# Optimization experiments

Hardware: AMD Instinct MI355X
Metric: run time of the kernel (lower is better)

Reference implementation:

```python
import jax, jax.numpy as jnp
import numpy as np


def setup_inputs() -> dict:
    key = jax.random.key(0)
    k1, k2, k3, k4 = jax.random.split(key, 4)
    N, M, D = 4096, 4096, 8
    x = jax.random.normal(k1, (N, D), dtype=jnp.float32)
    xx = jax.random.normal(k2, (M, D), dtype=jnp.float32)
    # raw (free-form) hyperparameters; positive() = softplus
    scale_raw = jax.random.normal(k3, (D,), dtype=jnp.float32)
    variance_raw = jax.random.normal(k4, (), dtype=jnp.float32)
    return {"x": x, "xx": xx, "scale_raw": scale_raw, "variance_raw": variance_raw}


def reference(x, xx, scale_raw, variance_raw):
    scale = jax.nn.softplus(scale_raw)          # (D,)
    variance = jax.nn.softplus(variance_raw)    # scalar
    xs = x / scale                               # (N, D)
    xxs = xx / scale                             # (M, D)
    # squared euclidean distance without materializing (N, M, D):
    # ||a-b||^2 = ||a||^2 + ||b||^2 - 2 a.b
    sq_x = jnp.sum(xs * xs, axis=-1)             # (N,)
    sq_xx = jnp.sum(xxs * xxs, axis=-1)          # (M,)
    cross = jnp.einsum("nd,md->nm", xs, xxs)    # (N, M)
    d2 = jnp.maximum(sq_x[:, None] + sq_xx[None, :] - 2.0 * cross, 0.0)
    cov = jnp.exp(-0.5 * d2) * variance          # (N, M)
    return cov
```

## Files before the change

kernel.cpp:

```cpp
#include <hip/hip_runtime.h>
#include <math.h>


#define TILE_N 16
#define BLOCK 256
#define D 8
#define M_PER_BLOCK (BLOCK * 4)

typedef float v2f __attribute__((ext_vector_type(2)));
typedef float v4f __attribute__((ext_vector_type(4)));

__device__ __forceinline__ float softplus_f(float z) {
    return fmaxf(z, 0.0f) + log1pf(__expf(-fabsf(z)));
}

__device__ __forceinline__ float fast_exp2(float z) {
    return __builtin_exp2f(z);
}

__global__ __launch_bounds__(BLOCK) void rbf_kernel(
    const float* __restrict__ x,
    const float* __restrict__ xx,
    const float* __restrict__ scale_raw,
    const float* __restrict__ var_raw,
    float* __restrict__ out,
    int N, int M)
{
    __shared__ float s_a[TILE_N][D];
    __shared__ float s_c[TILE_N];
    __shared__ float s_rs[D];
    __shared__ float s_l2v;

    const int tid = threadIdx.x;
    const int m0 = blockIdx.x * M_PER_BLOCK + tid * 4;
    const int n0 = blockIdx.y * TILE_N;

    if (tid < D) {
        s_rs[tid] = 1.2011224087864498f / softplus_f(scale_raw[tid]);
    }
    if (tid == D) {
        s_l2v = log2f(softplus_f(var_raw[0]));
    }
    __syncthreads();

    if (tid < TILE_N * D) {
        const int r = tid >> 3, c = tid & 7;
        s_a[r][c] = x[(n0 + r) * D + c] * s_rs[c];
    }

    float rs[D];
#pragma unroll
    for (int d = 0; d < D; ++d) rs[d] = s_rs[d];

    v2f b01[D], b23[D];
    {
        const float* xxp = xx + (size_t)m0 * D;
        float bj[4][D];
#pragma unroll
        for (int j = 0; j < 4; ++j) {
            const float4 lo = *(const float4*)(xxp + j * D);
            const float4 hi = *(const float4*)(xxp + j * D + 4);
            bj[j][0] = lo.x * rs[0]; bj[j][1] = lo.y * rs[1];
            bj[j][2] = lo.z * rs[2]; bj[j][3] = lo.w * rs[3];
            bj[j][4] = hi.x * rs[4]; bj[j][5] = hi.y * rs[5];
            bj[j][6] = hi.z * rs[6]; bj[j][7] = hi.w * rs[7];
        }
#pragma unroll
        for (int d = 0; d < D; ++d) {
            b01[d] = (v2f){bj[0][d], bj[1][d]};
            b23[d] = (v2f){bj[2][d], bj[3][d]};
        }
    }
    v2f h01 = {0.f, 0.f}, h23 = {0.f, 0.f};
#pragma unroll
    for (int d = 0; d < D; ++d) {
        h01 = __builtin_elementwise_fma(b01[d], b01[d], h01);
        h23 = __builtin_elementwise_fma(b23[d], b23[d], h23);
    }
    h01 *= 0.5f; h23 *= 0.5f;

    __syncthreads();

    if (tid < TILE_N) {
        float s = 0.f;
#pragma unroll
        for (int d = 0; d < D; ++d) s = fmaf(s_a[tid][d], s_a[tid][d], s);
        s_c[tid] = s_l2v - 0.5f * s;
    }
    __syncthreads();

    const float l2v = s_l2v;

#pragma unroll
    for (int n = 0; n < TILE_N; ++n) {
        const float4 alo = *(const float4*)&s_a[n][0];
        const float4 ahi = *(const float4*)&s_a[n][4];
        const float c = s_c[n];
        const float a_[D] = {alo.x, alo.y, alo.z, alo.w, ahi.x, ahi.y, ahi.z, ahi.w};

        v2f acc01 = (v2f){c, c} - h01;
        v2f acc23 = (v2f){c, c} - h23;
#pragma unroll
        for (int d = 0; d < D; ++d) {
            const v2f av = (v2f){a_[d], a_[d]};
            acc01 = __builtin_elementwise_fma(av, b01[d], acc01);
            acc23 = __builtin_elementwise_fma(av, b23[d], acc23);
        }

        v4f r;
        r.x = fast_exp2(fminf(acc01.x, l2v));
        r.y = fast_exp2(fminf(acc01.y, l2v));
        r.z = fast_exp2(fminf(acc23.x, l2v));
        r.w = fast_exp2(fminf(acc23.y, l2v));
        __builtin_nontemporal_store(r, (v4f*)(out + (size_t)(n0 + n) * M + m0));
    }
}

extern "C" void kernel_launch(void* const* d_in, const int* in_sizes, int n_in,
                              void* d_out, int out_size, void* d_ws, size_t ws_size,
                              hipStream_t stream) {
    const float* x    = (const float*)d_in[0];
    const float* xx   = (const float*)d_in[1];
    const float* sraw = (const float*)d_in[2];
    const float* vraw = (const float*)d_in[3];
    float* out = (float*)d_out;

    const int N = in_sizes[0] / D;
    const int M = in_sizes[1] / D;

    dim3 grid(M / M_PER_BLOCK, N / TILE_N);
    rbf_kernel<<<grid, BLOCK, 0, stream>>>(x, xx, sraw, vraw, out, N, M);
}
```

Baseline: 88.35 us.

## Reshape RBF tile to 8 rows x 8 columns per thread and drop a block barrier

Changes the per-thread tile from 4 columns by 16 rows to 8 columns by 8 rows, so each thread issues two contiguous float4 stores per row. Every thread now computes the softplus scales itself with fast hardware intrinsics, which removes the shared-memory broadcast and one __syncthreads. Row norms are computed in parallel with the row loading, and launch bounds ask for 4 blocks per CU. Register use goes up, and the store pattern has 32-byte strided chunks per thread instead of 16-byte ones, which may change how well writes coalesce.

```diff
diff --git a/kernel.cpp b/kernel.cpp
--- a/kernel.cpp
+++ b/kernel.cpp
@@ -2,23 +2,23 @@
 #include <math.h>
 
 
-#define TILE_N 16
+#define TILE_N 8
+#define D 8
 #define BLOCK 256
-#define D 8
-#define M_PER_BLOCK (BLOCK * 4)
+#define M_PER_T 8
+#define M_PER_BLOCK (BLOCK * M_PER_T)
 
 typedef float v2f __attribute__((ext_vector_type(2)));
 typedef float v4f __attribute__((ext_vector_type(4)));
 
-__device__ __forceinline__ float softplus_f(float z) {
-    return fmaxf(z, 0.0f) + log1pf(__expf(-fabsf(z)));
+__device__ __forceinline__ float fast_softplus(float z) {
+    const float LOG2E = 1.4426950408889634f;
+    const float LN2   = 0.6931471805599453f;
+    const float t = __builtin_amdgcn_exp2f(-fabsf(z) * LOG2E);
+    return fmaxf(z, 0.0f) + LN2 * __builtin_amdgcn_logf(1.0f + t);
 }
 
-__device__ __forceinline__ float fast_exp2(float z) {
-    return __builtin_exp2f(z);
-}
-
-__global__ __launch_bounds__(BLOCK) void rbf_kernel(
+__global__ __launch_bounds__(BLOCK, 4) void rbf_kernel(
     const float* __restrict__ x,
     const float* __restrict__ xx,
     const float* __restrict__ scale_raw,
@@ -28,91 +28,114 @@
 {
     __shared__ float s_a[TILE_N][D];
     __shared__ float s_c[TILE_N];
-    __shared__ float s_rs[D];
-    __shared__ float s_l2v;
 
     const int tid = threadIdx.x;
-    const int m0 = blockIdx.x * M_PER_BLOCK + tid * 4;
+    const int m0 = blockIdx.x * M_PER_BLOCK + tid * M_PER_T;
     const int n0 = blockIdx.y * TILE_N;
 
-    if (tid < D) {
-        s_rs[tid] = 1.2011224087864498f / softplus_f(scale_raw[tid]);
+    const float SQ_L2E = 1.2011224087864498f;
+
+    float rs[D];
+    {
+        const float4 s0 = *(const float4*)(scale_raw);
+        const float4 s1 = *(const float4*)(scale_raw + 4);
+        rs[0] = SQ_L2E * __builtin_amdgcn_rcpf(fast_softplus(s0.x));
+        rs[1] = SQ_L2E * __builtin_amdgcn_rcpf(fast_softplus(s0.y));
+        rs[2] = SQ_L2E * __builtin_amdgcn_rcpf(fast_softplus(s0.z));
+        rs[3] = SQ_L2E * __builtin_amdgcn_rcpf(fast_softplus(s0.w));
+        rs[4] = SQ_L2E * __builtin_amdgcn_rcpf(fast_softplus(s1.x));
+        rs[5] = SQ_L2E * __builtin_amdgcn_rcpf(fast_softplus(s1.y));
+        rs[6] = SQ_L2E * __builtin_amdgcn_rcpf(fast_softplus(s1.z));
+        rs[7] = SQ_L2E * __builtin_amdgcn_rcpf(fast_softplus(s1.w));
     }
-    if (tid == D) {
-        s_l2v = log2f(softplus_f(var_raw[0]));
-    }
-    __syncthreads();
+    const float l2v = __builtin_amdgcn_logf(fast_softplus(var_raw[0]));
 
     if (tid < TILE_N * D) {
         const int r = tid >> 3, c = tid & 7;
-        s_a[r][c] = x[(n0 + r) * D + c] * s_rs[c];
+        const float rsc = SQ_L2E * __builtin_amdgcn_rcpf(fast_softplus(scale_raw[c]));
+        s_a[r][c] = x[(n0 + r) * D + c] * rsc;
+    } else if (tid < TILE_N * D + TILE_N) {
+        const int r = tid - TILE_N * D;
+        const float4 lo = *(const float4*)(x + (size_t)(n0 + r) * D);
+        const float4 hi = *(const float4*)(x + (size_t)(n0 + r) * D + 4);
+        const float a0 = lo.x * rs[0], a1 = lo.y * rs[1];
+        const float a2 = lo.z * rs[2], a3 = lo.w * rs[3];
+        const float a4 = hi.x * rs[4], a5 = hi.y * rs[5];
+        const float a6 = hi.z * rs[6], a7 = hi.w * rs[7];
+        float s = a0 * a0;
+        s = fmaf(a1, a1, s); s = fmaf(a2, a2, s); s = fmaf(a3, a3, s);
+        s = fmaf(a4, a4, s); s = fmaf(a5, a5, s); s = fmaf(a6, a6, s);
+        s = fmaf(a7, a7, s);
+        s_c[r] = l2v - 0.5f * s;
     }
 
-    float rs[D];
-#pragma unroll
-    for (int d = 0; d < D; ++d) rs[d] = s_rs[d];
-
-    v2f b01[D], b23[D];
+    v2f b[4][D];
+    v2f h[4];
     {
         const float* xxp = xx + (size_t)m0 * D;
-        float bj[4][D];
 #pragma unroll
-        for (int j = 0; j < 4; ++j) {
-            const float4 lo = *(const float4*)(xxp + j * D);
-            const float4 hi = *(const float4*)(xxp + j * D + 4);
-            bj[j][0] = lo.x * rs[0]; bj[j][1] = lo.y * rs[1];
-            bj[j][2] = lo.z * rs[2]; bj[j][3] = lo.w * rs[3];
-            bj[j][4] = hi.x * rs[4]; bj[j][5] = hi.y * rs[5];
-            bj[j][6] = hi.z * rs[6]; bj[j][7] = hi.w * rs[7];
-        }
+        for (int p = 0; p < 4; ++p) {
+            const float4 e0 = *(const float4*)(xxp + (2 * p) * D);
+            const float4 e1 = *(const float4*)(xxp + (2 * p) * D + 4);
+            const float4 f0 = *(const float4*)(xxp + (2 * p + 1) * D);
+            const float4 f1 = *(const float4*)(xxp + (2 * p + 1) * D + 4);
+            b[p][0] = (v2f){e0.x, f0.x} * rs[0];
+            b[p][1] = (v2f){e0.y, f0.y} * rs[1];
+            b[p][2] = (v2f){e0.z, f0.z} * rs[2];
+            b[p][3] = (v2f){e0.w, f0.w} * rs[3];
+            b[p][4] = (v2f){e1.x, f1.x} * rs[4];
+            b[p][5] = (v2f){e1.y, f1.y} * rs[5];
+            b[p][6] = (v2f){e1.z, f1.z} * rs[6];
+            b[p][7] = (v2f){e1.w, f1.w} * rs[7];
+            v2f s = b[p][0] * b[p][0];
 #pragma unroll
-        for (int d = 0; d < D; ++d) {
-            b01[d] = (v2f){bj[0][d], bj[1][d]};
-            b23[d] = (v2f){bj[2][d], bj[3][d]};
+            for (int d = 1; d < D; ++d)
+                s = __builtin_elementwise_fma(b[p][d], b[p][d], s);
+            h[p] = s * 0.5f;
         }
     }
-    v2f h01 = {0.f, 0.f}, h23 = {0.f, 0.f};
-#pragma unroll
-    for (int d = 0; d < D; ++d) {
-        h01 = __builtin_elementwise_fma(b01[d], b01[d], h01);
-        h23 = __builtin_elementwise_fma(b23[d], b23[d], h23);
-    }
-    h01 *= 0.5f; h23 *= 0.5f;
 
     __syncthreads();
 
-    if (tid < TILE_N) {
-        float s = 0.f;
-#pragma unroll
-        for (int d = 0; d < D; ++d) s = fmaf(s_a[tid][d], s_a[tid][d], s);
-        s_c[tid] = s_l2v - 0.5f * s;
-    }
-    __syncthreads();
+    const float4 c03 = *(const float4*)&s_c[0];
+    const float4 c47 = *(const float4*)&s_c[4];
+    const float cn[TILE_N] = {c03.x, c03.y, c03.z, c03.w,
+                              c47.x, c47.y, c47.z, c47.w};
 
-    const float l2v = s_l2v;
-
+    float* orow = out + (size_t)n0 * M + m0;
 #pragma unroll
     for (int n = 0; n < TILE_N; ++n) {
         const float4 alo = *(const float4*)&s_a[n][0];
         const float4 ahi = *(const float4*)&s_a[n][4];
-        const float c = s_c[n];
-        const float a_[D] = {alo.x, alo.y, alo.z, alo.w, ahi.x, ahi.y, ahi.z, ahi.w};
+        const float a_[D] = {alo.x, alo.y, alo.z, alo.w,
+                             ahi.x, ahi.y, ahi.z, ahi.w};
+        const float c = cn[n];
 
-        v2f acc01 = (v2f){c, c} - h01;
-        v2f acc23 = (v2f){c, c} - h23;
+        v2f acc0 = (v2f){c, c} - h[0];
+        v2f acc1 = (v2f){c, c} - h[1];
+        v2f acc2 = (v2f){c, c} - h[2];
+        v2f acc3 = (v2f){c, c} - h[3];
 #pragma unroll
         for (int d = 0; d < D; ++d) {
             const v2f av = (v2f){a_[d], a_[d]};
-            acc01 = __builtin_elementwise_fma(av, b01[d], acc01);
-            acc23 = __builtin_elementwise_fma(av, b23[d], acc23);
+            acc0 = __builtin_elementwise_fma(av, b[0][d], acc0);
+            acc1 = __builtin_elementwise_fma(av, b[1][d], acc1);
+            acc2 = __builtin_elementwise_fma(av, b[2][d], acc2);
+            acc3 = __builtin_elementwise_fma(av, b[3][d], acc3);
         }
 
-        v4f r;
-        r.x = fast_exp2(fminf(acc01.x, l2v));
-        r.y = fast_exp2(fminf(acc01.y, l2v));
-        r.z = fast_exp2(fminf(acc23.x, l2v));
-        r.w = fast_exp2(fminf(acc23.y, l2v));
-        __builtin_nontemporal_store(r, (v4f*)(out + (size_t)(n0 + n) * M + m0));
+        v4f r0, r1;
+        r0.x = __builtin_amdgcn_exp2f(fminf(acc0.x, l2v));
+        r0.y = __builtin_amdgcn_exp2f(fminf(acc0.y, l2v));
+        r0.z = __builtin_amdgcn_exp2f(fminf(acc1.x, l2v));
+        r0.w = __builtin_amdgcn_exp2f(fminf(acc1.y, l2v));
+        r1.x = __builtin_amdgcn_exp2f(fminf(acc2.x, l2v));
+        r1.y = __builtin_amdgcn_exp2f(fminf(acc2.y, l2v));
+        r1.z = __builtin_amdgcn_exp2f(fminf(acc3.x, l2v));
+        r1.w = __builtin_amdgcn_exp2f(fminf(acc3.y, l2v));
+        __builtin_nontemporal_store(r0, (v4f*)orow);
+        __builtin_nontemporal_store(r1, (v4f*)(orow + 4));
+        orow += M;
     }
 }
 
```

Result: slower. 103.6 us (+17.3%).
